# Performance work log

Hardware: AMD Instinct MI355X
Metric: run time of the kernel (lower is better)

The kernel has to match this reference:

```python
import jax, jax.numpy as jnp
import numpy as np

NUM_STEPS = 32
HIDDEN = 1024
BATCH = 1024


def setup_inputs() -> dict:
    key = jax.random.key(0)
    ks = jax.random.split(key, 10)
    s = 1.0 / np.sqrt(HIDDEN)  # PyTorch LSTM/Linear init scale
    return {
        "in_data": jax.random.normal(ks[0], (BATCH, 1), dtype=jnp.float32),
        "batch_size": BATCH,
        "h0": jax.random.normal(ks[1], (1, BATCH, HIDDEN), dtype=jnp.float32),
        "c0": jax.random.normal(ks[2], (1, BATCH, HIDDEN), dtype=jnp.float32),
        # LSTM params (PyTorch layout: gates stacked [i, f, g, o])
        "W_ih": jax.random.uniform(ks[3], (4 * HIDDEN, 1), jnp.float32, -s, s),
        "W_hh": jax.random.uniform(ks[4], (4 * HIDDEN, HIDDEN), jnp.float32, -s, s),
        "b_ih": jax.random.uniform(ks[5], (4 * HIDDEN,), jnp.float32, -s, s),
        "b_hh": jax.random.uniform(ks[6], (4 * HIDDEN,), jnp.float32, -s, s),
        # output Linear(hidden_dim, 1)
        "W_out": jax.random.uniform(ks[7], (1, HIDDEN), jnp.float32, -s, s),
        "b_out": jax.random.uniform(ks[8], (1,), jnp.float32, -s, s),
    }


def reference(in_data, batch_size, h0, c0, W_ih, W_hh, b_ih, b_hh, W_out, b_out):
    # (seq_len=1) then Linear(H->1); the scalar output feeds back as next input.
    h = h0[0]  # (B, H)
    c = c0[0]  # (B, H)
    bias = b_ih + b_hh

    def step(carry, _):
        x, h, c = carry  # x: (B, 1)
        gates = x @ W_ih.T + h @ W_hh.T + bias  # (B, 4H)
        i, f, g, o = jnp.split(gates, 4, axis=-1)
        c_new = jax.nn.sigmoid(f) * c + jax.nn.sigmoid(i) * jnp.tanh(g)
        h_new = jax.nn.sigmoid(o) * jnp.tanh(c_new)
        y = h_new @ W_out.T + b_out  # (B, 1)
        return (y, h_new, c_new), y[:, 0]

    _, ys = jax.lax.scan(step, (in_data, h, c), None, length=NUM_STEPS)
    # ys: (num_steps, B) -> (B, num_steps), matching stack().squeeze(2).permute(1,0)
    return ys.T
```

## Files before the change

### kernel.cpp

```cpp
#include <hip/hip_runtime.h>

#define H 1024
#define FH 4096
#define T 32
#define HSZ (1u << 20)

typedef unsigned short u16;
typedef unsigned int u32;
typedef __attribute__((ext_vector_type(8))) short short8;
typedef __attribute__((ext_vector_type(4))) float f32x4;
typedef __attribute__((ext_vector_type(4))) u32 u32x4;

__device__ __forceinline__ u16 f2b(float f) {
    union { float f; u32 i; } x; x.f = f;
    u32 r = x.i + 0x7fff + ((x.i >> 16) & 1);
    return (u16)(r >> 16);
}
__device__ __forceinline__ float sigm(float x) {
    return __fdividef(1.f, 1.f + __expf(-x));
}
__device__ __forceinline__ float ftanh(float x) {
    float t = __expf(-2.f * fabsf(x));
    return copysignf(__fdividef(1.f - t, 1.f + t), x);
}

__global__ void prep_weff_k(const float* __restrict__ Whh, const float* __restrict__ Wih,
                            const float* __restrict__ Wo, u16* __restrict__ weff) {
    int idx = (blockIdx.x * 256 + threadIdx.x) * 8;
    int r = idx >> 10, k = idx & 1023;
    float wih = Wih[r];
    short8 outv;
#pragma unroll
    for (int e = 0; e < 8; e++) {
        float v = Whh[idx + e] + wih * Wo[k + e];
        outv[e] = (short)f2b(v);
    }
    *(short8*)(weff + idx) = outv;
}

__global__ void prep_misc_k(const float* __restrict__ h0, const float* __restrict__ bih,
                            const float* __restrict__ bhh, const float* __restrict__ bo,
                            const float* __restrict__ Wih,
                            u16* __restrict__ hbase, float* __restrict__ biasp,
                            float* __restrict__ out) {
    int i = (blockIdx.x * 256 + threadIdx.x) * 4;
#pragma unroll
    for (int e = 0; e < 4; e++) hbase[i + e] = f2b(h0[i + e]);
    if (blockIdx.x == 0) {
        for (int b = threadIdx.x; b < FH; b += 256)
            biasp[b] = bih[b] + bhh[b] + bo[0] * Wih[b];
    }
    if (blockIdx.x < 32) {
        float b0 = bo[0];
        int o = blockIdx.x * 1024 + threadIdx.x * 4;
#pragma unroll
        for (int e = 0; e < 4; e++) out[o + e] = b0;
    }
}

__global__ void prep_d0_k(const float* __restrict__ in_data, const float* __restrict__ h0,
                          const float* __restrict__ Wo, const float* __restrict__ bo,
                          float* __restrict__ dd0) {
    int lane = threadIdx.x & 63, wid = threadIdx.x >> 6;
    for (int rr = 0; rr < 4; ++rr) {
        int m = blockIdx.x * 16 + (wid << 2) + rr;
        const float* hp = h0 + ((u32)m << 10) + lane * 16;
        const float* wp = Wo + lane * 16;
        float s = 0.f;
#pragma unroll
        for (int e = 0; e < 16; e++) s += hp[e] * wp[e];
#pragma unroll
        for (int off = 32; off >= 1; off >>= 1) s += __shfl_xor(s, off, 64);
        if (lane == 0) dd0[m] = in_data[m] - s - bo[0];
    }
}

template<bool COH>
__global__ __launch_bounds__(512) void lstm_persist_k(
    const u16* __restrict__ weff, u16* __restrict__ hbase,
    const float* __restrict__ biasp, const float* __restrict__ dd0,
    const float* __restrict__ Wih, const float* __restrict__ Wo,
    const float* __restrict__ c0, float* __restrict__ out, u32* __restrict__ cnt)
{
    __shared__ __align__(16) char smem[67584];
    float* gb0 = (float*)smem;
    float* gb1 = (float*)(smem + 33792);

    const int tid = threadIdx.x;
    const int lane = tid & 63, wid = tid >> 6;
    const int kg = wid >> 2;
    const int wrr = (wid >> 1) & 1, wcc = wid & 1;
    const int bx = blockIdx.x;
    const int mb = (bx >> 3) & 7;
    const int jb = (bx & 7) * 4 + (bx >> 6);
    const int m0 = mb << 7, j0 = jb << 5;
    const int rl = lane & 15, sl = lane >> 4;
    const int jj = tid & 31, rgrp = tid >> 5;
    const int j = j0 + jj;

    const float bs0 = biasp[j], bs1 = biasp[H + j], bs2 = biasp[2*H + j], bs3 = biasp[3*H + j];
    const float wi0 = Wih[j], wi1 = Wih[H + j], wi2 = Wih[2*H + j], wi3 = Wih[3*H + j];
    const float woj = Wo[j];
    float c_reg[8];
#pragma unroll
    for (int p = 0; p < 2; ++p)
#pragma unroll
        for (int q = 0; q < 4; ++q)
            c_reg[p * 4 + q] = c0[(u32)(m0 + p * 64 + rgrp * 4 + q) * H + j];

    int arow[4], brow[4], koff[4], dstA[4], dstB[4];
#pragma unroll
    for (int i = 0; i < 4; i++) {
        int c_ = tid + i * 512;
        int row = c_ >> 4, cs = c_ & 15;
        koff[i] = (cs >> 3) * 512 + (cs & 7) * 8;
        arow[i] = m0 + row;
        brow[i] = ((row >> 5) << 10) + j0 + (row & 31);
        int dchunk = row * 16 + (cs ^ (row & 15));
        dstA[i] = dchunk * 16;
        dstB[i] = 32768 + dchunk * 16;
    }

    for (int s = 0; s < T; ++s) {
        const u16* hin = hbase + (u32)(COH ? (s & 1) : s) * HSZ;
        u16* hout      = hbase + (u32)(COH ? ((s + 1) & 1) : (s + 1)) * HSZ;

        f32x4 acc[4][4];
#pragma unroll
        for (int im = 0; im < 4; im++)
#pragma unroll
            for (int in_ = 0; in_ < 4; in_++) acc[im][in_] = (f32x4){0.f, 0.f, 0.f, 0.f};

        u32x4 ph[4], pw[4];
        auto loadt = [&](int it) {
#pragma unroll
            for (int i = 0; i < 4; i++) {
                const u16* pa = hin + ((u32)arow[i] << 10) + it * 64 + koff[i];
                const u16* pb = weff + ((u32)brow[i] << 10) + it * 64 + koff[i];
                if constexpr (COH) {
                    asm volatile("global_load_dwordx4 %0, %1, off sc0 sc1"
                                 : "=v"(ph[i]) : "v"(pa));
                } else {
                    ph[i] = *(const u32x4*)pa;
                }
                pw[i] = *(const u32x4*)pb;
            }
        };
        auto writet = [&]() {
            if constexpr (COH) {
                asm volatile("s_waitcnt vmcnt(0)" ::: "memory");
                __builtin_amdgcn_sched_barrier(0);
            }
#pragma unroll
            for (int i = 0; i < 4; i++) {
                *(u32x4*)(smem + dstA[i]) = ph[i];
                *(u32x4*)(smem + dstB[i]) = pw[i];
            }
        };

        loadt(0); writet();

        for (int it = 0; it < 8; ++it) {
            __syncthreads();
            if (it < 7) loadt(it + 1);
#pragma unroll
            for (int ks = 0; ks < 2; ++ks) {
                short8 af[4], bg[4];
#pragma unroll
                for (int im = 0; im < 4; ++im) {
                    int row = wrr * 64 + im * 16 + rl;
                    int sb = row * 256 + (((kg * 8 + ks * 4 + sl) * 16) ^ ((row & 15) << 4));
                    af[im] = *(const short8*)(smem + sb);
                }
#pragma unroll
                for (int in_ = 0; in_ < 4; ++in_) {
                    int n = wcc * 64 + in_ * 16 + rl;
                    int sb = 32768 + n * 256 + (((kg * 8 + ks * 4 + sl) * 16) ^ ((n & 15) << 4));
                    bg[in_] = *(const short8*)(smem + sb);
                }
#pragma unroll
                for (int im = 0; im < 4; ++im)
#pragma unroll
                    for (int in_ = 0; in_ < 4; ++in_)
                        acc[im][in_] = __builtin_amdgcn_mfma_f32_16x16x32_bf16(
                            af[im], bg[in_], acc[im][in_], 0, 0, 0);
            }
            __syncthreads();
            if (it < 7) writet();
        }

#pragma unroll
        for (int p = 0; p < 2; ++p) {
            __syncthreads();
            if (wrr == p) {
                float* g = kg ? gb1 : gb0;
#pragma unroll
                for (int im = 0; im < 4; ++im)
#pragma unroll
                    for (int in_ = 0; in_ < 4; ++in_)
#pragma unroll
                        for (int qq = 0; qq < 4; ++qq) {
                            int r = im * 16 + sl * 4 + qq;
                            g[r * 132 + wcc * 64 + in_ * 16 + rl] = acc[im][in_][qq];
                        }
            }
            __syncthreads();
#pragma unroll
            for (int q = 0; q < 4; ++q) {
                int rloc = rgrp * 4 + q;
                int m_abs = m0 + p * 64 + rloc;
                const float* g0 = gb0 + rloc * 132;
                const float* g1 = gb1 + rloc * 132;
                float gi  = g0[jj]      + g1[jj]      + bs0;
                float gf_ = g0[32 + jj] + g1[32 + jj] + bs1;
                float gg_ = g0[64 + jj] + g1[64 + jj] + bs2;
                float go_ = g0[96 + jj] + g1[96 + jj] + bs3;
                if (s == 0) {
                    float d = dd0[m_abs];
                    gi += d * wi0; gf_ += d * wi1; gg_ += d * wi2; go_ += d * wi3;
                }
                float cn = sigm(gf_) * c_reg[p * 4 + q] + sigm(gi) * ftanh(gg_);
                float hn = sigm(go_) * ftanh(cn);
                c_reg[p * 4 + q] = cn;

                if (s < T - 1) {
                    u32 hv = (u32)f2b(hn);
                    u32 nb = __shfl_down(hv, 1, 32);
                    if (!(jj & 1)) {
                        u32* hp = (u32*)(hout + (((u32)m_abs << 10) + j));
                        __hip_atomic_store(hp, (nb << 16) | hv,
                                           __ATOMIC_RELAXED, __HIP_MEMORY_SCOPE_AGENT);
                    }
                }
                float yp = hn * woj;
                yp += __shfl_xor(yp, 16, 32);
                yp += __shfl_xor(yp, 8, 32);
                yp += __shfl_xor(yp, 4, 32);
                yp += __shfl_xor(yp, 2, 32);
                yp += __shfl_xor(yp, 1, 32);
                if (jj == 0)
                    __hip_atomic_fetch_add(out + (u32)m_abs * T + s, yp,
                                           __ATOMIC_RELAXED, __HIP_MEMORY_SCOPE_AGENT);
            }
        }

        if (s < T - 1) {
            __syncthreads();
            if (tid == 0) {
                u32* cc = cnt + ((u32)(s * 8 + mb) << 4);
                __hip_atomic_fetch_add(cc, 1u, __ATOMIC_RELAXED, __HIP_MEMORY_SCOPE_AGENT);
                while (__hip_atomic_load(cc, __ATOMIC_RELAXED, __HIP_MEMORY_SCOPE_AGENT) < 32u)
                    __builtin_amdgcn_s_sleep(2);
            }
            __syncthreads();
        }
    }
}

extern "C" void kernel_launch(void* const* d_in, const int* in_sizes, int n_in,
                              void* d_out, int out_size, void* d_ws, size_t ws_size,
                              hipStream_t stream) {
    const float* in_data = (const float*)d_in[0];
    const float* h0  = (const float*)d_in[2];
    const float* c0  = (const float*)d_in[3];
    const float* Wih = (const float*)d_in[4];
    const float* Whh = (const float*)d_in[5];
    const float* bih = (const float*)d_in[6];
    const float* bhh = (const float*)d_in[7];
    const float* Wo  = (const float*)d_in[8];
    const float* bo  = (const float*)d_in[9];
    float* out = (float*)d_out;
    char* ws = (char*)d_ws;

    u16*   weff  = (u16*)ws;
    float* biasp = (float*)(ws + (8u << 20));
    float* dd0   = (float*)(ws + (8u << 20) + 16384);
    u32*   cnt   = (u32*)(ws + (8u << 20) + 24576);
    u16*   hbase = (u16*)(ws + (8u << 20) + 65536);

    bool rot = ws_size >= ((size_t)76 << 20);

    hipMemsetAsync(cnt, 0, 16384, stream);
    hipLaunchKernelGGL(prep_weff_k, dim3(2048), dim3(256), 0, stream, Whh, Wih, Wo, weff);
    hipLaunchKernelGGL(prep_misc_k, dim3(1024), dim3(256), 0, stream,
                       h0, bih, bhh, bo, Wih, hbase, biasp, out);
    hipLaunchKernelGGL(prep_d0_k, dim3(64), dim3(256), 0, stream, in_data, h0, Wo, bo, dd0);

    if (rot)
        hipLaunchKernelGGL((lstm_persist_k<false>), dim3(256), dim3(512), 0, stream,
                           weff, hbase, biasp, dd0, Wih, Wo, c0, out, cnt);
    else
        hipLaunchKernelGGL((lstm_persist_k<true>), dim3(256), dim3(512), 0, stream,
                           weff, hbase, biasp, dd0, Wih, Wo, c0, out, cnt);
}
```

Baseline: 511.9 us.

## Double-buffer LDS tiles, prefetch weight tile during barrier, single-pass gate epilogue

Shared memory grows to two 64KB buffers so each K-iteration computes from one buffer while the next tile is written to the other, removing the second __syncthreads per iteration. The first weight tile of the next step is loaded during the inter-block barrier wait, hiding it behind the spin. The gate epilogue now writes all accumulators at once into a swizzled layout and processes 8 rows per thread in one pass instead of two, and MFMA sections run at raised wave priority. The larger LDS footprint limits occupancy to one block per CU, and the swizzle and buffer reuse add correctness risk.

```diff
diff --git a/kernel.cpp b/kernel.cpp
--- a/kernel.cpp
+++ b/kernel.cpp
@@ -82,9 +82,7 @@
     const float* __restrict__ Wih, const float* __restrict__ Wo,
     const float* __restrict__ c0, float* __restrict__ out, u32* __restrict__ cnt)
 {
-    __shared__ __align__(16) char smem[67584];
-    float* gb0 = (float*)smem;
-    float* gb1 = (float*)(smem + 33792);
+    __shared__ __align__(16) char smem[131072];
 
     const int tid = threadIdx.x;
     const int lane = tid & 63, wid = tid >> 6;
@@ -103,10 +101,8 @@
     const float woj = Wo[j];
     float c_reg[8];
 #pragma unroll
-    for (int p = 0; p < 2; ++p)
-#pragma unroll
-        for (int q = 0; q < 4; ++q)
-            c_reg[p * 4 + q] = c0[(u32)(m0 + p * 64 + rgrp * 4 + q) * H + j];
+    for (int q = 0; q < 8; ++q)
+        c_reg[q] = c0[(u32)(m0 + rgrp * 8 + q) * H + j];
 
     int arow[4], brow[4], koff[4], dstA[4], dstB[4];
 #pragma unroll
@@ -132,37 +128,45 @@
             for (int in_ = 0; in_ < 4; in_++) acc[im][in_] = (f32x4){0.f, 0.f, 0.f, 0.f};
 
         u32x4 ph[4], pw[4];
-        auto loadt = [&](int it) {
+        auto loadA = [&](int it) {
 #pragma unroll
             for (int i = 0; i < 4; i++) {
                 const u16* pa = hin + ((u32)arow[i] << 10) + it * 64 + koff[i];
-                const u16* pb = weff + ((u32)brow[i] << 10) + it * 64 + koff[i];
                 if constexpr (COH) {
                     asm volatile("global_load_dwordx4 %0, %1, off sc0 sc1"
                                  : "=v"(ph[i]) : "v"(pa));
                 } else {
                     ph[i] = *(const u32x4*)pa;
                 }
-                pw[i] = *(const u32x4*)pb;
             }
         };
-        auto writet = [&]() {
+        auto loadB = [&](int it) {
+#pragma unroll
+            for (int i = 0; i < 4; i++)
+                pw[i] = *(const u32x4*)(weff + ((u32)brow[i] << 10) + it * 64 + koff[i]);
+        };
+        auto writeA = [&](int buf) {
             if constexpr (COH) {
                 asm volatile("s_waitcnt vmcnt(0)" ::: "memory");
                 __builtin_amdgcn_sched_barrier(0);
             }
 #pragma unroll
-            for (int i = 0; i < 4; i++) {
-                *(u32x4*)(smem + dstA[i]) = ph[i];
-                *(u32x4*)(smem + dstB[i]) = pw[i];
-            }
+            for (int i = 0; i < 4; i++) *(u32x4*)(smem + buf * 65536 + dstA[i]) = ph[i];
         };
-
-        loadt(0); writet();
+        auto writeB = [&](int buf) {
+#pragma unroll
+            for (int i = 0; i < 4; i++) *(u32x4*)(smem + buf * 65536 + dstB[i]) = pw[i];
+        };
+
+        if (s == 0) { loadB(0); writeB(0); }
+        loadA(0); writeA(0);
 
         for (int it = 0; it < 8; ++it) {
+            const int buf = it & 1;
             __syncthreads();
-            if (it < 7) loadt(it + 1);
+            if (it < 7) { loadA(it + 1); loadB(it + 1); }
+            const char* base = smem + buf * 65536;
+            __builtin_amdgcn_s_setprio(1);
 #pragma unroll
             for (int ks = 0; ks < 2; ++ks) {
                 short8 af[4], bg[4];
@@ -170,13 +174,13 @@
                 for (int im = 0; im < 4; ++im) {
                     int row = wrr * 64 + im * 16 + rl;
                     int sb = row * 256 + (((kg * 8 + ks * 4 + sl) * 16) ^ ((row & 15) << 4));
-                    af[im] = *(const short8*)(smem + sb);
+                    af[im] = *(const short8*)(base + sb);
                 }
 #pragma unroll
                 for (int in_ = 0; in_ < 4; ++in_) {
                     int n = wcc * 64 + in_ * 16 + rl;
                     int sb = 32768 + n * 256 + (((kg * 8 + ks * 4 + sl) * 16) ^ ((n & 15) << 4));
-                    bg[in_] = *(const short8*)(smem + sb);
+                    bg[in_] = *(const short8*)(base + sb);
                 }
 #pragma unroll
                 for (int im = 0; im < 4; ++im)
@@ -185,70 +189,74 @@
                         acc[im][in_] = __builtin_amdgcn_mfma_f32_16x16x32_bf16(
                             af[im], bg[in_], acc[im][in_], 0, 0, 0);
             }
-            __syncthreads();
-            if (it < 7) writet();
+            __builtin_amdgcn_s_setprio(0);
+            if (it < 7) { writeA(buf ^ 1); writeB(buf ^ 1); }
         }
 
-#pragma unroll
-        for (int p = 0; p < 2; ++p) {
-            __syncthreads();
-            if (wrr == p) {
-                float* g = kg ? gb1 : gb0;
-#pragma unroll
-                for (int im = 0; im < 4; ++im)
-#pragma unroll
-                    for (int in_ = 0; in_ < 4; ++in_)
-#pragma unroll
-                        for (int qq = 0; qq < 4; ++qq) {
-                            int r = im * 16 + sl * 4 + qq;
-                            g[r * 132 + wcc * 64 + in_ * 16 + rl] = acc[im][in_][qq];
-                        }
-            }
-            __syncthreads();
-#pragma unroll
-            for (int q = 0; q < 4; ++q) {
-                int rloc = rgrp * 4 + q;
-                int m_abs = m0 + p * 64 + rloc;
-                const float* g0 = gb0 + rloc * 132;
-                const float* g1 = gb1 + rloc * 132;
-                float gi  = g0[jj]      + g1[jj]      + bs0;
-                float gf_ = g0[32 + jj] + g1[32 + jj] + bs1;
-                float gg_ = g0[64 + jj] + g1[64 + jj] + bs2;
-                float go_ = g0[96 + jj] + g1[96 + jj] + bs3;
-                if (s == 0) {
-                    float d = dd0[m_abs];
-                    gi += d * wi0; gf_ += d * wi1; gg_ += d * wi2; go_ += d * wi3;
+        __syncthreads();
+        {
+            float* g = (float*)(smem + wrr * 65536 + kg * 32768);
+#pragma unroll
+            for (int im = 0; im < 4; ++im)
+#pragma unroll
+                for (int in_ = 0; in_ < 4; ++in_)
+#pragma unroll
+                    for (int qq = 0; qq < 4; ++qq) {
+                        int r = im * 16 + sl * 4 + qq;
+                        int col = wcc * 64 + in_ * 16 + rl;
+                        g[r * 128 + (col ^ ((r & 7) << 2))] = acc[im][in_][qq];
+                    }
+        }
+        __syncthreads();
+#pragma unroll
+        for (int q = 0; q < 8; ++q) {
+            int m_loc = rgrp * 8 + q;
+            int m_abs = m0 + m_loc;
+            const float* g0 = (const float*)(smem + (m_loc >> 6) * 65536);
+            const float* g1 = g0 + 8192;
+            int r = m_loc & 63;
+            int jx = jj ^ ((r & 7) << 2);
+            const float* r0 = g0 + r * 128;
+            const float* r1 = g1 + r * 128;
+            float gi  = r0[jx]      + r1[jx]      + bs0;
+            float gf_ = r0[32 + jx] + r1[32 + jx] + bs1;
+            float gg_ = r0[64 + jx] + r1[64 + jx] + bs2;
+            float go_ = r0[96 + jx] + r1[96 + jx] + bs3;
+            if (s == 0) {
+                float d = dd0[m_abs];
+                gi += d * wi0; gf_ += d * wi1; gg_ += d * wi2; go_ += d * wi3;
+            }
+            float cn = sigm(gf_) * c_reg[q] + sigm(gi) * ftanh(gg_);
+            float hn = sigm(go_) * ftanh(cn);
+            c_reg[q] = cn;
+
+            if (s < T - 1) {
+                u32 hv = (u32)f2b(hn);
+                u32 nb = __shfl_down(hv, 1, 32);
+                if (!(jj & 1)) {
+                    u32* hp = (u32*)(hout + (((u32)m_abs << 10) + j));
+                    __hip_atomic_store(hp, (nb << 16) | hv,
+                                       __ATOMIC_RELAXED, __HIP_MEMORY_SCOPE_AGENT);
                 }
-                float cn = sigm(gf_) * c_reg[p * 4 + q] + sigm(gi) * ftanh(gg_);
-                float hn = sigm(go_) * ftanh(cn);
-                c_reg[p * 4 + q] = cn;
-
-                if (s < T - 1) {
-                    u32 hv = (u32)f2b(hn);
-                    u32 nb = __shfl_down(hv, 1, 32);
-                    if (!(jj & 1)) {
-                        u32* hp = (u32*)(hout + (((u32)m_abs << 10) + j));
-                        __hip_atomic_store(hp, (nb << 16) | hv,
-                                           __ATOMIC_RELAXED, __HIP_MEMORY_SCOPE_AGENT);
-                    }
-                }
-                float yp = hn * woj;
-                yp += __shfl_xor(yp, 16, 32);
-                yp += __shfl_xor(yp, 8, 32);
-                yp += __shfl_xor(yp, 4, 32);
-                yp += __shfl_xor(yp, 2, 32);
-                yp += __shfl_xor(yp, 1, 32);
-                if (jj == 0)
-                    __hip_atomic_fetch_add(out + (u32)m_abs * T + s, yp,
-                                           __ATOMIC_RELAXED, __HIP_MEMORY_SCOPE_AGENT);
-            }
+            }
+            float yp = hn * woj;
+            yp += __shfl_xor(yp, 16, 32);
+            yp += __shfl_xor(yp, 8, 32);
+            yp += __shfl_xor(yp, 4, 32);
+            yp += __shfl_xor(yp, 2, 32);
+            yp += __shfl_xor(yp, 1, 32);
+            if (jj == 0)
+                __hip_atomic_fetch_add(out + (u32)m_abs * T + s, yp,
+                                       __ATOMIC_RELAXED, __HIP_MEMORY_SCOPE_AGENT);
         }
 
         if (s < T - 1) {
             __syncthreads();
+            u32* cc = cnt + ((u32)(s * 8 + mb) << 4);
+            if (tid == 0)
+                __hip_atomic_fetch_add(cc, 1u, __ATOMIC_RELAXED, __HIP_MEMORY_SCOPE_AGENT);
+            loadB(0); writeB(0);
             if (tid == 0) {
-                u32* cc = cnt + ((u32)(s * 8 + mb) << 4);
-                __hip_atomic_fetch_add(cc, 1u, __ATOMIC_RELAXED, __HIP_MEMORY_SCOPE_AGENT);
                 while (__hip_atomic_load(cc, __ATOMIC_RELAXED, __HIP_MEMORY_SCOPE_AGENT) < 32u)
                     __builtin_amdgcn_s_sleep(2);
             }
```

Result: slower. 1.170 ms (+128.7%).

## Pre-swizzle weights into MFMA fragment layout and load B directly from global

Applied to the files above, without the earlier changes.

The weight-prep kernel now writes the combined bf16 weight matrix in a fragment-major layout that matches the MFMA B-operand lane layout. The persistent LSTM kernel loads B fragments straight from global/L2 into registers, which removes the LDS staging stores, the swizzled LDS reads and half the shared traffic for the weights. In exchange, weight loads sit on the critical path each k-iteration without double-buffering through LDS, and every wave fetches its own fragments, so global load latency may be exposed.

```diff
diff --git a/kernel.cpp b/kernel.cpp
--- a/kernel.cpp
+++ b/kernel.cpp
@@ -25,17 +25,19 @@
 }
 
 __global__ void prep_weff_k(const float* __restrict__ Whh, const float* __restrict__ Wih,
-                            const float* __restrict__ Wo, u16* __restrict__ weff) {
-    int idx = (blockIdx.x * 256 + threadIdx.x) * 8;
-    int r = idx >> 10, k = idx & 1023;
+                            const float* __restrict__ Wo, u16* __restrict__ wf) {
+    int t = blockIdx.x * 256 + threadIdx.x;
+    int f = t >> 6, l = t & 63;
+    int gct = f >> 5, kstep = f & 31;
+    int r = gct * 16 + (l & 15);
+    int k0 = kstep * 32 + (l >> 4) * 8;
     float wih = Wih[r];
-    short8 outv;
-#pragma unroll
-    for (int e = 0; e < 8; e++) {
-        float v = Whh[idx + e] + wih * Wo[k + e];
-        outv[e] = (short)f2b(v);
-    }
-    *(short8*)(weff + idx) = outv;
+    const float* wr_ = Whh + (u32)r * H + k0;
+    const float* wo_ = Wo + k0;
+    short8 v;
+#pragma unroll
+    for (int e = 0; e < 8; e++) v[e] = (short)f2b(wr_[e] + wih * wo_[e]);
+    *(short8*)(wf + ((u32)f << 9) + l * 8) = v;
 }
 
 __global__ void prep_misc_k(const float* __restrict__ h0, const float* __restrict__ bih,
@@ -77,7 +79,7 @@
 
 template<bool COH>
 __global__ __launch_bounds__(512) void lstm_persist_k(
-    const u16* __restrict__ weff, u16* __restrict__ hbase,
+    const u16* __restrict__ wf, u16* __restrict__ hbase,
     const float* __restrict__ biasp, const float* __restrict__ dd0,
     const float* __restrict__ Wih, const float* __restrict__ Wo,
     const float* __restrict__ c0, float* __restrict__ out, u32* __restrict__ cnt)
@@ -108,17 +110,21 @@
         for (int q = 0; q < 4; ++q)
             c_reg[p * 4 + q] = c0[(u32)(m0 + p * 64 + rgrp * 4 + q) * H + j];
 
-    int arow[4], brow[4], koff[4], dstA[4], dstB[4];
+    int arow[4], koff[4], dstA[4];
 #pragma unroll
     for (int i = 0; i < 4; i++) {
         int c_ = tid + i * 512;
         int row = c_ >> 4, cs = c_ & 15;
         koff[i] = (cs >> 3) * 512 + (cs & 7) * 8;
         arow[i] = m0 + row;
-        brow[i] = ((row >> 5) << 10) + j0 + (row & 31);
-        int dchunk = row * 16 + (cs ^ (row & 15));
-        dstA[i] = dchunk * 16;
-        dstB[i] = 32768 + dchunk * 16;
+        dstA[i] = (row * 16 + (cs ^ (row & 15))) * 16;
+    }
+
+    int gct[4];
+#pragma unroll
+    for (int in_ = 0; in_ < 4; ++in_) {
+        int ctb = wcc * 4 + in_;
+        gct[in_] = (ctb >> 1) * 64 + jb * 2 + (ctb & 1);
     }
 
     for (int s = 0; s < T; ++s) {
@@ -131,41 +137,44 @@
 #pragma unroll
             for (int in_ = 0; in_ < 4; in_++) acc[im][in_] = (f32x4){0.f, 0.f, 0.f, 0.f};
 
-        u32x4 ph[4], pw[4];
-        auto loadt = [&](int it) {
+        u32x4 ph[4];
+        auto loadA = [&](int it) {
 #pragma unroll
             for (int i = 0; i < 4; i++) {
                 const u16* pa = hin + ((u32)arow[i] << 10) + it * 64 + koff[i];
-                const u16* pb = weff + ((u32)brow[i] << 10) + it * 64 + koff[i];
                 if constexpr (COH) {
                     asm volatile("global_load_dwordx4 %0, %1, off sc0 sc1"
                                  : "=v"(ph[i]) : "v"(pa));
                 } else {
                     ph[i] = *(const u32x4*)pa;
                 }
-                pw[i] = *(const u32x4*)pb;
             }
         };
-        auto writet = [&]() {
+        auto writeA = [&]() {
             if constexpr (COH) {
                 asm volatile("s_waitcnt vmcnt(0)" ::: "memory");
                 __builtin_amdgcn_sched_barrier(0);
             }
 #pragma unroll
-            for (int i = 0; i < 4; i++) {
-                *(u32x4*)(smem + dstA[i]) = ph[i];
-                *(u32x4*)(smem + dstB[i]) = pw[i];
-            }
+            for (int i = 0; i < 4; i++) *(u32x4*)(smem + dstA[i]) = ph[i];
         };
 
-        loadt(0); writet();
+        loadA(0); writeA();
 
         for (int it = 0; it < 8; ++it) {
             __syncthreads();
-            if (it < 7) loadt(it + 1);
+            short8 bg[2][4];
+#pragma unroll
+            for (int ks = 0; ks < 2; ++ks)
+#pragma unroll
+                for (int in_ = 0; in_ < 4; ++in_) {
+                    u32 fidx = (u32)(gct[in_] * 32 + kg * 16 + it * 2 + ks);
+                    bg[ks][in_] = *(const short8*)(wf + (fidx << 9) + lane * 8);
+                }
+            if (it < 7) loadA(it + 1);
 #pragma unroll
             for (int ks = 0; ks < 2; ++ks) {
-                short8 af[4], bg[4];
+                short8 af[4];
 #pragma unroll
                 for (int im = 0; im < 4; ++im) {
                     int row = wrr * 64 + im * 16 + rl;
@@ -173,20 +182,14 @@
                     af[im] = *(const short8*)(smem + sb);
                 }
 #pragma unroll
-                for (int in_ = 0; in_ < 4; ++in_) {
-                    int n = wcc * 64 + in_ * 16 + rl;
-                    int sb = 32768 + n * 256 + (((kg * 8 + ks * 4 + sl) * 16) ^ ((n & 15) << 4));
-                    bg[in_] = *(const short8*)(smem + sb);
-                }
-#pragma unroll
                 for (int im = 0; im < 4; ++im)
 #pragma unroll
                     for (int in_ = 0; in_ < 4; ++in_)
                         acc[im][in_] = __builtin_amdgcn_mfma_f32_16x16x32_bf16(
-                            af[im], bg[in_], acc[im][in_], 0, 0, 0);
-            }
-            __syncthreads();
-            if (it < 7) writet();
+                            af[im], bg[ks][in_], acc[im][in_], 0, 0, 0);
+            }
+            __syncthreads();
+            if (it < 7) writeA();
         }
 
 #pragma unroll
```

After: 509.9 us. Within noise of the previous version (-0.4%).
